# Kernel optimization log

Measured on AMD Instinct MI355X. Metric: run time of the kernel, lower is better.

The kernel has to match this reference:

```python
import jax, jax.numpy as jnp
import numpy as np

N_NODES = 50000
N_EDGES = 800000
IN_FEATS = 256
H_FEATS = 256
NUM_CLASSES = 16
NUM_GRAPHS = 64


def _glorot(key, shape):
    lim = float(np.sqrt(6.0 / (shape[0] + shape[1])))
    return jax.random.uniform(key, shape, jnp.float32, -lim, lim)


def setup_inputs() -> dict:
    key = jax.random.key(0)
    ks = jax.random.split(key, 12)
    x = jax.random.normal(ks[0], (N_NODES, IN_FEATS), jnp.float32)
    edge_index = jax.random.randint(ks[1], (2, N_EDGES), 0, N_NODES, jnp.int64)
    batch_vec = jnp.sort(jax.random.randint(ks[2], (N_NODES,), 0, NUM_GRAPHS, jnp.int64))
    W1 = _glorot(ks[3], (IN_FEATS, H_FEATS)); b1 = jnp.zeros((H_FEATS,), jnp.float32)
    W2 = _glorot(ks[4], (H_FEATS, H_FEATS)); b2 = jnp.zeros((H_FEATS,), jnp.float32)
    W3 = _glorot(ks[5], (H_FEATS, H_FEATS)); b3 = jnp.zeros((H_FEATS,), jnp.float32)
    W4 = _glorot(ks[6], (H_FEATS, NUM_CLASSES)); b4 = jnp.zeros((NUM_CLASSES,), jnp.float32)
    return {"x": x, "edge_index": edge_index, "batch_vec": batch_vec,
            "W1": W1, "b1": b1, "W2": W2, "b2": b2,
            "W3": W3, "b3": b3, "W4": W4, "b4": b4}


def gcn_conv(x, W, b, src, dst, deg_inv_sqrt):
    # PyG GCNConv: out = D^{-1/2} (A + I) D^{-1/2} (x W) + b
    h = x @ W  # [N, F_out]
    norm = deg_inv_sqrt[src] * deg_inv_sqrt[dst]  # [E+N]
    msgs = h[src] * norm[:, None]  # gather + scale
    agg = jax.ops.segment_sum(msgs, dst, num_segments=x.shape[0])
    return agg + b


def reference(x, edge_index, batch_vec, W1, b1, W2, b2, W3, b3, W4, b4):
    n = x.shape[0]
    # add self-loops once (shared across layers)
    loops = jnp.arange(n, dtype=edge_index.dtype)
    src = jnp.concatenate([edge_index[0], loops])
    dst = jnp.concatenate([edge_index[1], loops])
    deg = jax.ops.segment_sum(jnp.ones_like(dst, dtype=x.dtype), dst, num_segments=n)
    deg_inv_sqrt = jnp.where(deg > 0, jax.lax.rsqrt(deg), 0.0)

    h = gcn_conv(x, W1, b1, src, dst, deg_inv_sqrt)
    h_copy = jax.nn.relu(h)
    # dropout is identity in eval mode (training=False)
    h = gcn_conv(h_copy, W2, b2, src, dst, deg_inv_sqrt)
    h_copy = jax.nn.relu(jax.nn.relu(h) + h_copy)
    h = gcn_conv(h_copy, W3, b3, src, dst, deg_inv_sqrt)
    h = jax.nn.relu(jax.nn.relu(h) + h_copy)
    h = gcn_conv(h, W4, b4, src, dst, deg_inv_sqrt)

    # global_mean_pool over batch vector
    sums = jax.ops.segment_sum(h, batch_vec, num_segments=NUM_GRAPHS)
    counts = jax.ops.segment_sum(jnp.ones((n,), h.dtype), batch_vec, num_segments=NUM_GRAPHS)
    return sums / jnp.maximum(counts, 1.0)[:, None]
```

## Files before the change

kernel.cpp:

```cpp
#include <hip/hip_runtime.h>
#include <hip/hip_bf16.h>

#define N_NODES 50000
#define N_EDGES 800000
#define F 256
#define NGRAPH 64
#define NCLS 16
#define NBLK_N 196

typedef short short8 __attribute__((ext_vector_type(8)));
typedef float f32x4 __attribute__((ext_vector_type(4)));

__device__ __forceinline__ float bf2f(ushort u) {
    unsigned v = ((unsigned)u) << 16;
    return __uint_as_float(v);
}
__device__ __forceinline__ ushort f2bf(float f) {
    __hip_bfloat16 b = __float2bfloat16(f);
    return *reinterpret_cast<ushort*>(&b);
}
__device__ __forceinline__ float bflo(uint u) { return __uint_as_float(u << 16); }
__device__ __forceinline__ float bfhi(uint u) { return __uint_as_float(u & 0xffff0000u); }


__global__ __launch_bounds__(256) void k_init(int* __restrict__ ecnt,
                                              float* __restrict__ pool,
                                              float* __restrict__ cnt) {
    int i = blockIdx.x * 256 + threadIdx.x;
    if (i < N_NODES) ecnt[i] = 0;
    if (i < NGRAPH * NCLS) pool[i] = 0.f;
    if (i < NGRAPH) cnt[i] = 0.f;
}

__global__ __launch_bounds__(256) void k_count(const int* __restrict__ dst,
                                               int* __restrict__ ecnt) {
    int e = blockIdx.x * 256 + threadIdx.x;
    if (e < N_EDGES) atomicAdd(&ecnt[dst[e]], 1);
}

__global__ __launch_bounds__(256) void k_scan_block(const int* __restrict__ ecnt,
                                                    int* __restrict__ rowptr,
                                                    int* __restrict__ blkSum,
                                                    float* __restrict__ dinv) {
    __shared__ int sh[256];
    int i = blockIdx.x * 256 + threadIdx.x;
    int v = (i < N_NODES) ? ecnt[i] : 0;
    sh[threadIdx.x] = v;
    __syncthreads();
#pragma unroll
    for (int off = 1; off < 256; off <<= 1) {
        int t = (threadIdx.x >= off) ? sh[threadIdx.x - off] : 0;
        __syncthreads();
        sh[threadIdx.x] += t;
        __syncthreads();
    }
    if (i < N_NODES) {
        rowptr[i] = sh[threadIdx.x] - v;
        dinv[i] = rsqrtf((float)(v + 1));
    }
    if (threadIdx.x == 255) blkSum[blockIdx.x] = sh[255];
}

__global__ __launch_bounds__(256) void k_scan_add(const int* __restrict__ blkSum,
                                                  int* __restrict__ rowptr,
                                                  int* __restrict__ cursor) {
    __shared__ int sh[256];
    int t = threadIdx.x;
    sh[t] = (t < NBLK_N && t < (int)blockIdx.x) ? blkSum[t] : 0;
    __syncthreads();
#pragma unroll
    for (int off = 128; off > 0; off >>= 1) {
        if (t < off) sh[t] += sh[t + off];
        __syncthreads();
    }
    int base = sh[0];
    int i = blockIdx.x * 256 + t;
    if (i < N_NODES) {
        int r = rowptr[i] + base;
        rowptr[i] = r;
        cursor[i] = r;
    }
    if (i == 0) rowptr[N_NODES] = N_EDGES;
}

__global__ __launch_bounds__(256) void k_fill_csr(const int* __restrict__ src,
                                                  const int* __restrict__ dst,
                                                  int* __restrict__ cursor,
                                                  ushort* __restrict__ csr16) {
    int e = blockIdx.x * 256 + threadIdx.x;
    if (e >= N_EDGES) return;
    int s = src[e];
    int d = dst[e];
    int p = atomicAdd(&cursor[d], 1);
    csr16[p] = (ushort)s;
}


__global__ __launch_bounds__(256) void k_wpack3(const float* __restrict__ W1,
                                                const float* __restrict__ W2,
                                                const float* __restrict__ W3,
                                                ushort* __restrict__ Wp) {
    int gid = blockIdx.x * 256 + threadIdx.x;
    int which = gid >> 13;
    int idx = gid & 8191;
    const float* W = (which == 0) ? W1 : (which == 1) ? W2 : W3;
    ushort* o = Wp + (size_t)which * 65536;
    int lane = idx & 63;
    int ks = (idx >> 6) & 7;
    int ctg = idx >> 9;
    int kbase = ks * 32 + (lane >> 4) * 8;
    int col = ctg * 16 + (lane & 15);
    short8 v;
#pragma unroll
    for (int e = 0; e < 8; ++e)
        v[e] = (short)f2bf(W[(size_t)(kbase + e) * 256 + col]);
    *(short8*)(o + (size_t)idx * 8) = v;
}


template <int F32IN>
__global__ __launch_bounds__(256, 2) void k_mfma256(const void* __restrict__ Av,
                                                    const ushort* __restrict__ Wp,
                                                    const float* __restrict__ dinv,
                                                    ushort* __restrict__ C) {
    __shared__ __align__(16) ushort cs[4][16 * 64];
    const int t = threadIdx.x;
    const int wv = t >> 6;
    const int l = t & 63;
    const int m0 = blockIdx.x * 64;
    const int colbase = wv * 64;
    const int lrow = l & 15;
    const int lk = (l >> 4) * 8;

    short8 wf[4][8];
    const short8* wp = (const short8*)Wp;
#pragma unroll
    for (int ct = 0; ct < 4; ++ct)
#pragma unroll
        for (int ks = 0; ks < 8; ++ks)
            wf[ct][ks] = wp[(size_t)(((wv * 4 + ct) * 8 + ks) * 64) + l];

#pragma unroll
    for (int msub = 0; msub < 4; ++msub) {
        int arow = m0 + msub * 16 + lrow;
        if (arow >= N_NODES) arow = N_NODES - 1;
        short8 af[8];
        if (F32IN) {
            const float* ap = (const float*)Av + (size_t)arow * F + lk;
#pragma unroll
            for (int ks = 0; ks < 8; ++ks) {
                float4 a0 = *(const float4*)(ap + ks * 32);
                float4 a1 = *(const float4*)(ap + ks * 32 + 4);
                af[ks][0] = (short)f2bf(a0.x); af[ks][1] = (short)f2bf(a0.y);
                af[ks][2] = (short)f2bf(a0.z); af[ks][3] = (short)f2bf(a0.w);
                af[ks][4] = (short)f2bf(a1.x); af[ks][5] = (short)f2bf(a1.y);
                af[ks][6] = (short)f2bf(a1.z); af[ks][7] = (short)f2bf(a1.w);
            }
        } else {
            const ushort* ap = (const ushort*)Av + (size_t)arow * F + lk;
#pragma unroll
            for (int ks = 0; ks < 8; ++ks)
                af[ks] = *(const short8*)(ap + ks * 32);
        }

        f32x4 acc[4];
#pragma unroll
        for (int ct = 0; ct < 4; ++ct) acc[ct] = (f32x4){0.f, 0.f, 0.f, 0.f};
#pragma unroll
        for (int ks = 0; ks < 8; ++ks)
#pragma unroll
            for (int ct = 0; ct < 4; ++ct)
                acc[ct] = __builtin_amdgcn_mfma_f32_16x16x32_bf16(af[ks], wf[ct][ks], acc[ct], 0, 0, 0);

        int orow0 = m0 + msub * 16 + (l >> 4) * 4;
        float dv[4];
#pragma unroll
        for (int r = 0; r < 4; ++r)
            dv[r] = (orow0 + r < N_NODES) ? dinv[orow0 + r] : 0.f;

#pragma unroll
        for (int ct = 0; ct < 4; ++ct) {
            int col = ct * 16 + (l & 15);
#pragma unroll
            for (int r = 0; r < 4; ++r) {
                int row = (l >> 4) * 4 + r;
                cs[wv][row * 64 + col] = f2bf(acc[ct][r] * dv[r]);
            }
        }
#pragma unroll
        for (int h = 0; h < 2; ++h) {
            int row = h * 8 + (l >> 3);
            int coff = (l & 7) * 8;
            short8 v = *(const short8*)&cs[wv][row * 64 + coff];
            int orow = m0 + msub * 16 + row;
            if (orow < N_NODES)
                *(short8*)(C + (size_t)orow * F + colbase + coff) = v;
        }
    }
}


template <int MODE>
__global__ __launch_bounds__(256) void k_gather256(const ushort* __restrict__ H,
                                                   const float* __restrict__ bias,
                                                   const float* __restrict__ dinv,
                                                   const int* __restrict__ rowptr,
                                                   const ushort* __restrict__ csr16,
                                                   const ushort* __restrict__ hc,
                                                   ushort* __restrict__ OUT) {
    int gid = blockIdx.x * 256 + threadIdx.x;
    int n = gid >> 6;
    int lane = gid & 63;
    if (n >= N_NODES) return;
    const int slot = lane >> 5;
    const int c = (lane & 31) * 8;

    float acc[8];
#pragma unroll
    for (int j = 0; j < 8; ++j) acc[j] = 0.f;

    int i = rowptr[n] + slot;
    const int end = rowptr[n + 1];
    for (; i + 6 < end; i += 8) {
        int s0 = csr16[i], s1 = csr16[i + 2], s2 = csr16[i + 4], s3 = csr16[i + 6];
        short8 v0 = *(const short8*)(H + (size_t)s0 * F + c);
        short8 v1 = *(const short8*)(H + (size_t)s1 * F + c);
        short8 v2 = *(const short8*)(H + (size_t)s2 * F + c);
        short8 v3 = *(const short8*)(H + (size_t)s3 * F + c);
#pragma unroll
        for (int j = 0; j < 8; ++j)
            acc[j] += (bf2f((ushort)v0[j]) + bf2f((ushort)v1[j])) +
                      (bf2f((ushort)v2[j]) + bf2f((ushort)v3[j]));
    }
    for (; i < end; i += 2) {
        int s0 = csr16[i];
        short8 v0 = *(const short8*)(H + (size_t)s0 * F + c);
#pragma unroll
        for (int j = 0; j < 8; ++j) acc[j] += bf2f((ushort)v0[j]);
    }

#pragma unroll
    for (int j = 0; j < 8; ++j) acc[j] += __shfl_xor(acc[j], 32);

    if (slot == 0) {
        const short8 h = *(const short8*)(H + (size_t)n * F + c);
        const float4 b0 = *(const float4*)(bias + c);
        const float4 b1 = *(const float4*)(bias + c + 4);
        float bb[8] = {b0.x, b0.y, b0.z, b0.w, b1.x, b1.y, b1.z, b1.w};
        float di = dinv[n];
        float s[8];
#pragma unroll
        for (int j = 0; j < 8; ++j)
            s[j] = bb[j] + di * (acc[j] + bf2f((ushort)h[j]));

        short8 ov;
        if (MODE == 1) {
#pragma unroll
            for (int j = 0; j < 8; ++j)
                ov[j] = (short)f2bf(fmaxf(s[j], 0.f));
        } else {
            const short8 hv = *(const short8*)(hc + (size_t)n * F + c);
#pragma unroll
            for (int j = 0; j < 8; ++j)
                ov[j] = (short)f2bf(fmaxf(fmaxf(s[j], 0.f) + bf2f((ushort)hv[j]), 0.f));
        }
        *(short8*)(OUT + (size_t)n * F + c) = ov;
    }
}


__global__ __launch_bounds__(256) void k_gemm16(const ushort* __restrict__ A,
                                                const float* __restrict__ W4,
                                                const float* __restrict__ dinv,
                                                ushort* __restrict__ C) {
    __shared__ float Ws[256][16];
    const int t = threadIdx.x;
    {
        const float4* wp = (const float4*)(W4 + (size_t)t * 16);
        float4 a = wp[0], b = wp[1], c = wp[2], d = wp[3];
        float4* sp = (float4*)&Ws[t][0];
        sp[0] = a; sp[1] = b; sp[2] = c; sp[3] = d;
    }
    __syncthreads();
    int row = blockIdx.x * 256 + t;
    if (row >= N_NODES) return;
    const short8* ap = (const short8*)(A + (size_t)row * F);
    float acc[16];
#pragma unroll
    for (int c = 0; c < 16; ++c) acc[c] = 0.f;
    for (int k8 = 0; k8 < 32; ++k8) {
        short8 a8 = ap[k8];
#pragma unroll
        for (int j = 0; j < 8; ++j) {
            float av = bf2f((ushort)a8[j]);
            const float4* wr = (const float4*)&Ws[k8 * 8 + j][0];
            float4 w0 = wr[0], w1 = wr[1], w2 = wr[2], w3 = wr[3];
            acc[0]  += av * w0.x; acc[1]  += av * w0.y;
            acc[2]  += av * w0.z; acc[3]  += av * w0.w;
            acc[4]  += av * w1.x; acc[5]  += av * w1.y;
            acc[6]  += av * w1.z; acc[7]  += av * w1.w;
            acc[8]  += av * w2.x; acc[9]  += av * w2.y;
            acc[10] += av * w2.z; acc[11] += av * w2.w;
            acc[12] += av * w3.x; acc[13] += av * w3.y;
            acc[14] += av * w3.z; acc[15] += av * w3.w;
        }
    }
    float dv = dinv[row];
    short8 o0, o1;
#pragma unroll
    for (int c = 0; c < 8; ++c) o0[c] = (short)f2bf(acc[c] * dv);
#pragma unroll
    for (int c = 0; c < 8; ++c) o1[c] = (short)f2bf(acc[8 + c] * dv);
    short8* op = (short8*)(C + (size_t)row * 16);
    op[0] = o0; op[1] = o1;
}


__global__ __launch_bounds__(256) void k_g16pool(const ushort* __restrict__ G16,
                                                 const float* __restrict__ bias,
                                                 const float* __restrict__ dinv,
                                                 const int* __restrict__ rowptr,
                                                 const ushort* __restrict__ csr16,
                                                 const int* __restrict__ batch,
                                                 float* __restrict__ pool,
                                                 float* __restrict__ cnt) {
    __shared__ float ps[NGRAPH][NCLS];
    __shared__ float pc[NGRAPH];
    for (int i = threadIdx.x; i < NGRAPH * NCLS; i += 256) ((float*)ps)[i] = 0.f;
    if (threadIdx.x < NGRAPH) pc[threadIdx.x] = 0.f;
    __syncthreads();

    int gid = blockIdx.x * 256 + threadIdx.x;
    int n = gid >> 2;
    int q = (gid & 3) * 4;
    if (n < N_NODES) {
        float ax = 0.f, ay = 0.f, az = 0.f, aw = 0.f;
        const int end = rowptr[n + 1];
        for (int i = rowptr[n]; i < end; ++i) {
            int s0 = csr16[i];
            const uint2 u = *(const uint2*)(G16 + (size_t)s0 * 16 + q);
            ax += bflo(u.x); ay += bfhi(u.x);
            az += bflo(u.y); aw += bfhi(u.y);
        }
        const uint2 hu = *(const uint2*)(G16 + (size_t)n * 16 + q);
        const float4 b = *(const float4*)(bias + q);
        float di = dinv[n];
        int g = batch[n];
        atomicAdd(&ps[g][q + 0], b.x + di * (ax + bflo(hu.x)));
        atomicAdd(&ps[g][q + 1], b.y + di * (ay + bfhi(hu.x)));
        atomicAdd(&ps[g][q + 2], b.z + di * (az + bflo(hu.y)));
        atomicAdd(&ps[g][q + 3], b.w + di * (aw + bfhi(hu.y)));
        if ((gid & 3) == 0) atomicAdd(&pc[g], 1.f);
    }
    __syncthreads();

    for (int i = threadIdx.x; i < NGRAPH * NCLS; i += 256) {
        float v = ((float*)ps)[i];
        if (v != 0.f) unsafeAtomicAdd(&pool[i], v);
    }
    if (threadIdx.x < NGRAPH) {
        float v = pc[threadIdx.x];
        if (v > 0.f) unsafeAtomicAdd(&cnt[threadIdx.x], v);
    }
}

__global__ __launch_bounds__(256) void k_final(const float* __restrict__ pool,
                                               const float* __restrict__ cnt,
                                               float* __restrict__ out) {
    int i = blockIdx.x * 256 + threadIdx.x;
    if (i < NGRAPH * NCLS) out[i] = pool[i] / fmaxf(cnt[i >> 4], 1.f);
}


extern "C" void kernel_launch(void* const* d_in, const int* in_sizes, int n_in,
                              void* d_out, int out_size, void* d_ws, size_t ws_size,
                              hipStream_t stream) {
    const float* x   = (const float*)d_in[0];
    const int*   ei  = (const int*)d_in[1];
    const int*   bvec= (const int*)d_in[2];
    const float* W1  = (const float*)d_in[3];
    const float* b1  = (const float*)d_in[4];
    const float* W2  = (const float*)d_in[5];
    const float* b2  = (const float*)d_in[6];
    const float* W3  = (const float*)d_in[7];
    const float* b3  = (const float*)d_in[8];
    const float* W4  = (const float*)d_in[9];
    const float* b4  = (const float*)d_in[10];
    float* out = (float*)d_out;

    const int* src = ei;
    const int* dst = ei + N_EDGES;

    const size_t NF = (size_t)N_NODES * F;
    ushort* P   = (ushort*)d_ws;
    ushort* Q   = P + NF;
    ushort* Hg  = Q + NF;
    ushort* G16 = Hg + NF;
    float*  aux = (float*)(G16 + (size_t)N_NODES * 16 + 64);
    int*    ecnt   = (int*)aux;
    float*  dinv   = aux + N_NODES;
    int*    rowptr = (int*)(aux + 2 * N_NODES);
    int*    cursor = (int*)(aux + 3 * N_NODES + 64);
    int*    blkSum = (int*)(aux + 4 * N_NODES + 64);
    ushort* csr16  = (ushort*)(blkSum + 256);
    float*  pool   = (float*)(csr16 + N_EDGES);
    float*  cnt    = pool + NGRAPH * NCLS;
    ushort* Wp     = (ushort*)(cnt + NGRAPH);

    const int BN = NBLK_N;
    const int BE = (N_EDGES + 255) / 256;
    const int BM = (N_NODES + 63) / 64;
    const int BG = (N_NODES * 64 + 255) / 256;
    const int B4 = (N_NODES * 4 + 255) / 256;

    k_init<<<BN, 256, 0, stream>>>(ecnt, pool, cnt);
    k_count<<<BE, 256, 0, stream>>>(dst, ecnt);
    k_scan_block<<<BN, 256, 0, stream>>>(ecnt, rowptr, blkSum, dinv);
    k_scan_add<<<BN, 256, 0, stream>>>(blkSum, rowptr, cursor);
    k_fill_csr<<<BE, 256, 0, stream>>>(src, dst, cursor, csr16);

    k_wpack3<<<96, 256, 0, stream>>>(W1, W2, W3, Wp);

    k_mfma256<1><<<BM, 256, 0, stream>>>(x, Wp, dinv, Hg);
    k_gather256<1><<<BG, 256, 0, stream>>>(Hg, b1, dinv, rowptr, csr16, nullptr, P);

    k_mfma256<0><<<BM, 256, 0, stream>>>(P, Wp + 65536, dinv, Hg);
    k_gather256<2><<<BG, 256, 0, stream>>>(Hg, b2, dinv, rowptr, csr16, P, Q);

    k_mfma256<0><<<BM, 256, 0, stream>>>(Q, Wp + 131072, dinv, Hg);
    k_gather256<2><<<BG, 256, 0, stream>>>(Hg, b3, dinv, rowptr, csr16, Q, P);

    k_gemm16<<<BN, 256, 0, stream>>>(P, W4, dinv, G16);
    k_g16pool<<<B4, 256, 0, stream>>>(G16, b4, dinv, rowptr, csr16, bvec, pool, cnt);

    k_final<<<4, 256, 0, stream>>>(pool, cnt, out);
}
```

Baseline: 402.1 us.

## Split MFMA GEMM across 8 waves with shared-memory full-row output staging

The dense GEMM kernel now uses 512 threads (8 waves), each owning 32 output columns instead of 64. That halves per-wave weight registers and accumulators. The output tile is staged in one padded shared buffer covering full 256-column rows, so stores are full-row coalesced. The cost is two block-wide barriers per 16-row sub-tile, and each A row fragment is now loaded by twice as many waves.

```diff
diff --git a/kernel.cpp b/kernel.cpp
--- a/kernel.cpp
+++ b/kernel.cpp
@@ -119,26 +119,25 @@
 
 
 template <int F32IN>
-__global__ __launch_bounds__(256, 2) void k_mfma256(const void* __restrict__ Av,
-                                                    const ushort* __restrict__ Wp,
-                                                    const float* __restrict__ dinv,
-                                                    ushort* __restrict__ C) {
-    __shared__ __align__(16) ushort cs[4][16 * 64];
+__global__ __launch_bounds__(512) void k_mfma256(const void* __restrict__ Av,
+                                                 const ushort* __restrict__ Wp,
+                                                 const float* __restrict__ dinv,
+                                                 ushort* __restrict__ C) {
+    __shared__ __align__(16) ushort cs[16 * 264];
     const int t = threadIdx.x;
     const int wv = t >> 6;
     const int l = t & 63;
     const int m0 = blockIdx.x * 64;
-    const int colbase = wv * 64;
     const int lrow = l & 15;
     const int lk = (l >> 4) * 8;
 
-    short8 wf[4][8];
+    short8 wf[2][8];
     const short8* wp = (const short8*)Wp;
 #pragma unroll
-    for (int ct = 0; ct < 4; ++ct)
+    for (int c2 = 0; c2 < 2; ++c2)
 #pragma unroll
         for (int ks = 0; ks < 8; ++ks)
-            wf[ct][ks] = wp[(size_t)(((wv * 4 + ct) * 8 + ks) * 64) + l];
+            wf[c2][ks] = wp[(size_t)(((2 * wv + c2) * 8 + ks) * 64) + l];
 
 #pragma unroll
     for (int msub = 0; msub < 4; ++msub) {
@@ -163,39 +162,42 @@
                 af[ks] = *(const short8*)(ap + ks * 32);
         }
 
-        f32x4 acc[4];
-#pragma unroll
-        for (int ct = 0; ct < 4; ++ct) acc[ct] = (f32x4){0.f, 0.f, 0.f, 0.f};
-#pragma unroll
-        for (int ks = 0; ks < 8; ++ks)
-#pragma unroll
-            for (int ct = 0; ct < 4; ++ct)
-                acc[ct] = __builtin_amdgcn_mfma_f32_16x16x32_bf16(af[ks], wf[ct][ks], acc[ct], 0, 0, 0);
-
-        int orow0 = m0 + msub * 16 + (l >> 4) * 4;
+        f32x4 acc[2];
+        acc[0] = (f32x4){0.f, 0.f, 0.f, 0.f};
+        acc[1] = (f32x4){0.f, 0.f, 0.f, 0.f};
+#pragma unroll
+        for (int ks = 0; ks < 8; ++ks) {
+            acc[0] = __builtin_amdgcn_mfma_f32_16x16x32_bf16(af[ks], wf[0][ks], acc[0], 0, 0, 0);
+            acc[1] = __builtin_amdgcn_mfma_f32_16x16x32_bf16(af[ks], wf[1][ks], acc[1], 0, 0, 0);
+        }
+
+        int orow0 = msub * 16 + (l >> 4) * 4;
         float dv[4];
 #pragma unroll
-        for (int r = 0; r < 4; ++r)
-            dv[r] = (orow0 + r < N_NODES) ? dinv[orow0 + r] : 0.f;
-
-#pragma unroll
-        for (int ct = 0; ct < 4; ++ct) {
-            int col = ct * 16 + (l & 15);
+        for (int r = 0; r < 4; ++r) {
+            int gr = m0 + orow0 + r;
+            dv[r] = (gr < N_NODES) ? dinv[gr] : 0.f;
+        }
+
+#pragma unroll
+        for (int c2 = 0; c2 < 2; ++c2) {
+            int col = (2 * wv + c2) * 16 + (l & 15);
 #pragma unroll
             for (int r = 0; r < 4; ++r) {
                 int row = (l >> 4) * 4 + r;
-                cs[wv][row * 64 + col] = f2bf(acc[ct][r] * dv[r]);
+                cs[row * 264 + col] = f2bf(acc[c2][r] * dv[r]);
             }
         }
-#pragma unroll
-        for (int h = 0; h < 2; ++h) {
-            int row = h * 8 + (l >> 3);
-            int coff = (l & 7) * 8;
-            short8 v = *(const short8*)&cs[wv][row * 64 + coff];
+        __syncthreads();
+        {
+            int row = t >> 5;
+            int coff = (t & 31) * 8;
+            short8 v = *(const short8*)&cs[row * 264 + coff];
             int orow = m0 + msub * 16 + row;
             if (orow < N_NODES)
-                *(short8*)(C + (size_t)orow * F + colbase + coff) = v;
-        }
+                *(short8*)(C + (size_t)orow * F + coff) = v;
+        }
+        __syncthreads();
     }
 }
 
@@ -421,13 +423,13 @@
 
     k_wpack3<<<96, 256, 0, stream>>>(W1, W2, W3, Wp);
 
-    k_mfma256<1><<<BM, 256, 0, stream>>>(x, Wp, dinv, Hg);
+    k_mfma256<1><<<BM, 512, 0, stream>>>(x, Wp, dinv, Hg);
     k_gather256<1><<<BG, 256, 0, stream>>>(Hg, b1, dinv, rowptr, csr16, nullptr, P);
 
-    k_mfma256<0><<<BM, 256, 0, stream>>>(P, Wp + 65536, dinv, Hg);
+    k_mfma256<0><<<BM, 512, 0, stream>>>(P, Wp + 65536, dinv, Hg);
     k_gather256<2><<<BG, 256, 0, stream>>>(Hg, b2, dinv, rowptr, csr16, P, Q);
 
-    k_mfma256<0><<<BM, 256, 0, stream>>>(Q, Wp + 131072, dinv, Hg);
+    k_mfma256<0><<<BM, 512, 0, stream>>>(Q, Wp + 131072, dinv, Hg);
     k_gather256<2><<<BG, 256, 0, stream>>>(Hg, b3, dinv, rowptr, csr16, Q, P);
 
     k_gemm16<<<BN, 256, 0, stream>>>(P, W4, dinv, G16);
```

Result: slower. 458.4 us (+14.0%).
